# Performance work log

Measured on AMD Instinct MI355X. Metric: run time of the kernel, lower is better.

## Reference

```python
import jax, jax.numpy as jnp
import numpy as np
from jax import lax

K_NBR = 9  # K nearest neighbors
R = 2      # shuffle_scale


def pixel_unshuffle(x, r):
    B, C, H, W = x.shape
    x = x.reshape(B, C, H // r, r, W // r, r)
    return x.transpose(0, 1, 3, 5, 2, 4).reshape(B, C * r * r, H // r, W // r)


def pixel_shuffle(x, r):
    B, C, H, W = x.shape
    x = x.reshape(B, C // (r * r), r, r, H, W)
    return x.transpose(0, 1, 4, 2, 5, 3).reshape(B, C // (r * r), H * r, W * r)


def conv2d_same(x, w, b):
    y = lax.conv_general_dilated(x, w, (1, 1), 'SAME',
                                 dimension_numbers=('NCHW', 'OIHW', 'NCHW'))
    return y + b[None, :, None, None]


def convnn_branching_layer(x, idx, wa, ba, wb, bb, wp, bp):
    """Conv2d_ConvNN_Random_Branching with shuffle_pattern='BA'."""
    x = pixel_unshuffle(x, R)                      # (B, C*r^2, H/r, W/r)
    B, C, H, W = x.shape
    T = H * W
    # Branch 1: standard 3x3 conv
    y1 = conv2d_same(x, wa, ba)                    # (B, c1, H, W)
    # Branch 2: ConvNN on K nearest of N random samples
    xt = x.reshape(B, C, T)                        # tokens
    samp = xt[:, :, idx]                           # (B, C, N) random samples
    dots = jnp.einsum('bct,bcn->btn', xt, samp)
    xn = jnp.sum(xt * xt, axis=1)[:, :, None]      # (B, T, 1)
    sn = jnp.sum(samp * samp, axis=1)[:, None, :]  # (B, 1, N)
    dist = xn + sn - 2.0 * dots                    # squared euclidean (B, T, N)
    nbr = lax.top_k(-dist, K_NBR)[1]               # (B, T, K) indices into samples
    # gather neighbor features: (B, C, T*K)
    g = jnp.take_along_axis(samp, nbr.reshape(B, 1, T * K_NBR), axis=2)
    g = g.reshape(B, C, T, K_NBR)
    # Conv1d(kernel=K, stride=K) over stacked neighbors
    y2 = jnp.einsum('bctk,ock->bot', g, wb) + bb[None, :, None]
    y2 = y2.reshape(B, wb.shape[0], H, W)          # (B, c2, H, W)
    y = jax.nn.relu(jnp.concatenate([y1, y2], axis=1))
    y = conv2d_same(y, wp, bp)                     # 1x1 -> out*r^2 channels
    return pixel_shuffle(y, R)                     # (B, out, H*r, W*r)


def setup_inputs() -> dict:
    key = jax.random.key(0)
    ks = jax.random.split(key, 24)
    s = 0.02
    B = 256
    inp = {
        'x': jax.random.normal(ks[0], (B, 3, 32, 32), jnp.float32),
        'idx1': jax.random.randint(ks[1], (64,), 0, 256, jnp.int32),
        'idx2': jax.random.randint(ks[2], (64,), 0, 256, jnp.int32),
        # layer 1: Cin = 3*4 = 12, branches 16+16, out 16*4 = 64 pre-shuffle
        'w1a': jax.random.normal(ks[3], (16, 12, 3, 3), jnp.float32) * s,
        'b1a': jnp.zeros((16,), jnp.float32),
        'w1b': jax.random.normal(ks[4], (16, 12, 9), jnp.float32) * s,
        'b1b': jnp.zeros((16,), jnp.float32),
        'w1p': jax.random.normal(ks[5], (64, 32, 1, 1), jnp.float32) * s,
        'b1p': jnp.zeros((64,), jnp.float32),
        # layer 2: Cin = 16*4 = 64, branches 32+32, out 32*4 = 128 pre-shuffle
        'w2a': jax.random.normal(ks[6], (32, 64, 3, 3), jnp.float32) * s,
        'b2a': jnp.zeros((32,), jnp.float32),
        'w2b': jax.random.normal(ks[7], (32, 64, 9), jnp.float32) * s,
        'b2b': jnp.zeros((32,), jnp.float32),
        'w2p': jax.random.normal(ks[8], (128, 64, 1, 1), jnp.float32) * s,
        'b2p': jnp.zeros((128,), jnp.float32),
        # FC head
        'fc1w': jax.random.normal(ks[9], (1024, 32768), jnp.float32) * s,
        'fc1b': jnp.zeros((1024,), jnp.float32),
        'fc2w': jax.random.normal(ks[10], (10, 1024), jnp.float32) * s,
        'fc2b': jnp.zeros((10,), jnp.float32),
    }
    return inp


def reference(x, idx1, idx2, w1a, b1a, w1b, b1b, w1p, b1p,
              w2a, b2a, w2b, b2b, w2p, b2p, fc1w, fc1b, fc2w, fc2b):
    h = convnn_branching_layer(x, idx1, w1a, b1a, w1b, b1b, w1p, b1p)  # (B,16,32,32)
    h = convnn_branching_layer(h, idx2, w2a, b2a, w2b, b2b, w2p, b2p)  # (B,32,32,32)
    h = h.reshape(h.shape[0], -1)                   # (B, 32768)
    h = jax.nn.relu(h @ fc1w.T + fc1b)
    return h @ fc2w.T + fc2b                        # (B, num_classes)
```

## Files before the change

kernel.cpp:

```cpp
#include <hip/hip_runtime.h>
#include <cstdint>
#include <cstddef>


#define DI static __device__ __forceinline__

typedef __attribute__((ext_vector_type(8))) short short8;
typedef __attribute__((ext_vector_type(4))) float f32x4;

DI unsigned short f2bf(float v) {
  return __builtin_bit_cast(unsigned short, (__bf16)v);
}
DI float bf2f(unsigned short h) {
  return (float)__builtin_bit_cast(__bf16, h);
}

DI float xu1_at(const float* __restrict__ x, int b, int c, int t) {
  int h = t >> 4, w = t & 15;
  return x[(((size_t)b * 3 + (c >> 2)) * 32 + 2 * h + ((c >> 1) & 1)) * 32 + 2 * w + (c & 1)];
}

__global__ __launch_bounds__(256) void k_prepw(
    const float* __restrict__ w1b, float* __restrict__ wT1,
    const float* __restrict__ w2b, float* __restrict__ wT2,
    const float* __restrict__ w1p, float* __restrict__ wp1T,
    const float* __restrict__ w2p, float* __restrict__ wp2T,
    const float* __restrict__ w1a, float* __restrict__ wa1T,
    const float* __restrict__ w2a, float* __restrict__ wa2T)
{
  int i = blockIdx.x * 256 + threadIdx.x;
  if (i < 1728) {
    int k = i / 192, r = i % 192, c = r >> 4, o = r & 15;
    wT1[i] = w1b[((size_t)o * 12 + c) * 9 + k];
    return;
  }
  i -= 1728;
  if (i < 18432) {
    int k = i / 2048, r = i % 2048, c = r >> 5, o = r & 31;
    wT2[i] = w2b[((size_t)o * 64 + c) * 9 + k];
    return;
  }
  i -= 18432;
  if (i < 2048) { int ic = i >> 6, o = i & 63; wp1T[i] = w1p[(size_t)o * 32 + ic]; return; }
  i -= 2048;
  if (i < 8192) { int ic = i >> 7, o = i & 127; wp2T[i] = w2p[(size_t)o * 64 + ic]; return; }
  i -= 8192;
  if (i < 1728) {
    int o = i & 15, u = i >> 4, ic = u / 9, tp = u % 9;
    wa1T[i] = w1a[((size_t)o * 12 + ic) * 9 + tp];
    return;
  }
  i -= 1728;
  if (i < 18432) {
    int o = i & 31, u = i >> 5, ic = u / 9, tp = u % 9;
    wa2T[i] = w2a[((size_t)o * 64 + ic) * 9 + tp];
  }
}

template <int CIN, bool GATHER, int CCTOT, int OCT>
__global__ __launch_bounds__(256) void k_conv3x3(
    const float* __restrict__ xsrc, const float* __restrict__ xu,
    const float* __restrict__ waT, const float* __restrict__ bias,
    float* __restrict__ ycat)
{
  int b = blockIdx.x;
  int ocb = blockIdx.y * 16;
  __shared__ float xs[CIN * 256];
  int t = threadIdx.x;
  if (GATHER) {
    for (int i = t; i < CIN * 256; i += 256) {
      int c = i >> 8, tt = i & 255;
      xs[i] = xu1_at(xsrc, b, c, tt);
    }
  } else {
    for (int i = t; i < CIN * 256; i += 256) xs[i] = xu[(size_t)b * CIN * 256 + i];
  }
  __syncthreads();
  int tt = t & 127, og = t >> 7;
  int oc0 = ocb + og * 8;
  int h0 = tt >> 4, wc = tt & 15;
  float acc0[8], acc1[8];
#pragma unroll
  for (int o = 0; o < 8; ++o) { acc0[o] = bias[oc0 + o]; acc1[o] = acc0[o]; }
  bool vw0 = wc > 0, vw2 = wc < 15, vh0 = h0 > 0, vh7 = h0 < 7;
  bool m0v[9] = {vh0 && vw0, vh0, vh0 && vw2, vw0, true, vw2, vw0, true, vw2};
  bool m1v[9] = {vw0, true, vw2, vw0, true, vw2, vh7 && vw0, vh7, vh7 && vw2};
  int tc0[9], tc1[9];
#pragma unroll
  for (int dh = 0; dh < 3; ++dh)
#pragma unroll
    for (int dw = 0; dw < 3; ++dw) {
      int o0 = (h0 + dh - 1) * 16 + (wc + dw - 1);
      int o1 = (h0 + 8 + dh - 1) * 16 + (wc + dw - 1);
      tc0[dh * 3 + dw] = o0 < 0 ? 0 : (o0 > 255 ? 255 : o0);
      tc1[dh * 3 + dw] = o1 < 0 ? 0 : (o1 > 255 ? 255 : o1);
    }
#pragma unroll 2
  for (int ic = 0; ic < CIN; ++ic) {
    float xv0[9], xv1[9];
#pragma unroll
    for (int tp = 0; tp < 9; ++tp) {
      float v0 = xs[ic * 256 + tc0[tp]];
      float v1 = xs[ic * 256 + tc1[tp]];
      xv0[tp] = m0v[tp] ? v0 : 0.f;
      xv1[tp] = m1v[tp] ? v1 : 0.f;
    }
#pragma unroll
    for (int tp = 0; tp < 9; ++tp) {
      const float* wp = waT + ((size_t)ic * 9 + tp) * OCT + oc0;
      float4 wA = *(const float4*)wp;
      float4 wB = *(const float4*)(wp + 4);
      float wv[8] = {wA.x, wA.y, wA.z, wA.w, wB.x, wB.y, wB.z, wB.w};
#pragma unroll
      for (int o = 0; o < 8; ++o) {
        acc0[o] = fmaf(xv0[tp], wv[o], acc0[o]);
        acc1[o] = fmaf(xv1[tp], wv[o], acc1[o]);
      }
    }
  }
#pragma unroll
  for (int o = 0; o < 8; ++o) {
    ycat[((size_t)b * CCTOT + oc0 + o) * 256 + tt] = fmaxf(acc0[o], 0.f);
    ycat[((size_t)b * CCTOT + oc0 + o) * 256 + tt + 128] = fmaxf(acc1[o], 0.f);
  }
}

template <int C, bool GATHER, int OPT, int OTOT, int CCTOT, int OCBASE>
__global__ __launch_bounds__(256) void k_knn(
    const float* __restrict__ xsrc, const float* __restrict__ xu,
    const int* __restrict__ idx,
    const float* __restrict__ wT,
    const float* __restrict__ bb,
    float* __restrict__ ycat)
{
  int b = blockIdx.x, t = threadIdx.x;
  __shared__ float sph[C * 64];
  __shared__ float snvs[64];
  __shared__ int idxs[64];
  __shared__ int nbs[9 * 256];
  if (t < 64) idxs[t] = idx[t];
  __syncthreads();
  for (int i = t; i < C * 64; i += 256) {
    int c = i >> 6, n = i & 63;
    int p = idxs[n];
    sph[i] = GATHER ? xu1_at(xsrc, b, c, p) : xu[((size_t)b * C + c) * 256 + p];
  }
  __syncthreads();
  if (t < 64) {
    float s;
    {
#pragma clang fp contract(off)
      s = 0.f;
      for (int c = 0; c < C; ++c) { float v = sph[c * 64 + t]; s += v * v; }
    }
    snvs[t] = s;
  }
  float xcol[C];
#pragma unroll
  for (int c = 0; c < C; ++c)
    xcol[c] = GATHER ? xu1_at(xsrc, b, c, t) : xu[((size_t)b * C + c) * 256 + t];
  float xn;
  {
#pragma clang fp contract(off)
    xn = 0.f;
#pragma unroll
    for (int c = 0; c < C; ++c) xn += xcol[c] * xcol[c];
  }
  __syncthreads();
  float bd[9];
  int bn[9];
#pragma unroll
  for (int i = 0; i < 9; ++i) { bd[i] = __builtin_inff(); bn[i] = 1 << 30; }
#pragma unroll 1
  for (int n = 0; n < 64; ++n) {
    float snvn = snvs[n];
    float d;
    {
#pragma clang fp contract(off)
      float dot = 0.f;
#pragma unroll
      for (int c = 0; c < C; ++c) dot = fmaf(xcol[c], sph[c * 64 + n], dot);
      d = (xn + snvn) - 2.f * dot;
    }
    if (d < bd[8] || (d == bd[8] && n < bn[8])) {
      float dc = d;
      int nc = n;
#pragma unroll
      for (int i = 0; i < 9; ++i) {
        bool sw = (dc < bd[i]) || (dc == bd[i] && nc < bn[i]);
        float ob = bd[i]; int on = bn[i];
        bd[i] = sw ? dc : ob; bn[i] = sw ? nc : on;
        dc = sw ? ob : dc;   nc = sw ? on : nc;
      }
    }
  }
#pragma unroll
  for (int k = 0; k < 9; ++k) nbs[k * 256 + t] = bn[k];
  __syncthreads();
  int tt = t & 127, og = t >> 7;
  int o0 = og * OPT;
  int bnA[9], bnB[9];
#pragma unroll
  for (int k = 0; k < 9; ++k) {
    bnA[k] = nbs[k * 256 + tt];
    bnB[k] = nbs[k * 256 + tt + 128];
  }
  float acc0[OPT], acc1[OPT];
#pragma unroll
  for (int o = 0; o < OPT; ++o) { acc0[o] = bb[o0 + o]; acc1[o] = acc0[o]; }
#pragma unroll 1
  for (int k = 0; k < 9; ++k) {
    int n0 = bnA[k], n1 = bnB[k];
#pragma unroll 2
    for (int c = 0; c < C; ++c) {
      float sv0 = sph[c * 64 + n0];
      float sv1 = sph[c * 64 + n1];
      const float* wp = wT + ((size_t)k * C + c) * OTOT + o0;
#pragma unroll
      for (int oq = 0; oq < OPT / 4; ++oq) {
        float4 wv = ((const float4*)wp)[oq];
        float w4[4] = {wv.x, wv.y, wv.z, wv.w};
#pragma unroll
        for (int j = 0; j < 4; ++j) {
          acc0[oq * 4 + j] = fmaf(sv0, w4[j], acc0[oq * 4 + j]);
          acc1[oq * 4 + j] = fmaf(sv1, w4[j], acc1[oq * 4 + j]);
        }
      }
    }
  }
#pragma unroll
  for (int o = 0; o < OPT; ++o) {
    ycat[((size_t)b * CCTOT + OCBASE + o0 + o) * 256 + tt] = fmaxf(acc0[o], 0.f);
    ycat[((size_t)b * CCTOT + OCBASE + o0 + o) * 256 + tt + 128] = fmaxf(acc1[o], 0.f);
  }
}

template <int CIN, int OPT, int OCTOT, bool SHUF>
__global__ __launch_bounds__(256) void k_conv1x1(
    const float* __restrict__ yin, const float* __restrict__ wpT,
    const float* __restrict__ bias, float* __restrict__ out)
{
  int b = blockIdx.x, ocb = blockIdx.y * 2 * OPT, t = threadIdx.x;
  int tt = t & 127, og = t >> 7;
  int o0 = ocb + og * OPT;
  __shared__ float ys[CIN * 256];
  for (int i = t; i < CIN * 256; i += 256) ys[i] = yin[(size_t)b * CIN * 256 + i];
  __syncthreads();
  float acc0[OPT], acc1[OPT];
#pragma unroll
  for (int o = 0; o < OPT; ++o) { acc0[o] = bias[o0 + o]; acc1[o] = acc0[o]; }
#pragma unroll 2
  for (int ic = 0; ic < CIN; ++ic) {
    float sv0 = ys[ic * 256 + tt];
    float sv1 = ys[ic * 256 + tt + 128];
    const float* wp = wpT + (size_t)ic * OCTOT + o0;
#pragma unroll
    for (int oq = 0; oq < OPT / 4; ++oq) {
      float4 wv = ((const float4*)wp)[oq];
      float w4[4] = {wv.x, wv.y, wv.z, wv.w};
#pragma unroll
      for (int j = 0; j < 4; ++j) {
        acc0[oq * 4 + j] = fmaf(sv0, w4[j], acc0[oq * 4 + j]);
        acc1[oq * 4 + j] = fmaf(sv1, w4[j], acc1[oq * 4 + j]);
      }
    }
  }
  int h0 = tt >> 4, wc = tt & 15;
#pragma unroll
  for (int o = 0; o < OPT; ++o) {
    int ogl = o0 + o;
    if (SHUF) {
      int f0 = (ogl >> 2) * 1024 + (2 * h0 + ((ogl >> 1) & 1)) * 32 + (2 * wc + (ogl & 1));
      int f1 = (ogl >> 2) * 1024 + (2 * (h0 + 8) + ((ogl >> 1) & 1)) * 32 + (2 * wc + (ogl & 1));
      out[(size_t)b * 32768 + f0] = acc0[o];
      out[(size_t)b * 32768 + f1] = acc1[o];
    } else {
      out[((size_t)b * OCTOT + ogl) * 256 + tt] = acc0[o];
      out[((size_t)b * OCTOT + ogl) * 256 + tt + 128] = acc1[o];
    }
  }
}

__global__ __launch_bounds__(256, 2) void k_fc1(
    const float* __restrict__ A, const float* __restrict__ W,
    float* __restrict__ parts)
{
  constexpr int KTOT = 32768;
  constexpr int LDT = 36;
  __shared__ unsigned short Ah[128 * LDT], Am[128 * LDT], Al[128 * LDT];
  int t = threadIdx.x;
  int nb = blockIdx.x, mb = blockIdx.y, sb = blockIdx.z;
  int m0 = mb * 128, n0 = nb * 128, k0 = sb * 1024;
  int wave = t >> 6, lane = t & 63;
  int q = lane >> 4, m16 = lane & 15;

  f32x4 acc[8][2];
#pragma unroll
  for (int mt = 0; mt < 8; ++mt)
#pragma unroll
    for (int nt = 0; nt < 2; ++nt) acc[mt][nt] = (f32x4){0.f, 0.f, 0.f, 0.f};

  int arow = t >> 1, acol = (t & 1) * 16;
  const float* Ap = A + (size_t)(m0 + arow) * KTOT + k0 + acol;
  const float* W0 = W + (size_t)(n0 + wave * 32 + m16) * KTOT + k0 + q * 8;
  const float* W1 = W + (size_t)(n0 + wave * 32 + 16 + m16) * KTOT + k0 + q * 8;

  float4 aR0 = *(const float4*)(Ap + 0);
  float4 aR1 = *(const float4*)(Ap + 4);
  float4 aR2 = *(const float4*)(Ap + 8);
  float4 aR3 = *(const float4*)(Ap + 12);
  float4 w0a = *(const float4*)(W0), w0b = *(const float4*)(W0 + 4);
  float4 w1a = *(const float4*)(W1), w1b = *(const float4*)(W1 + 4);

  for (int ks = 0; ks < 1024; ks += 32) {
    int ksn = (ks + 32 < 1024) ? ks + 32 : 0;
    float4 nA0 = *(const float4*)(Ap + ksn);
    float4 nA1 = *(const float4*)(Ap + ksn + 4);
    float4 nA2 = *(const float4*)(Ap + ksn + 8);
    float4 nA3 = *(const float4*)(Ap + ksn + 12);
    float4 nW0a = *(const float4*)(W0 + ksn), nW0b = *(const float4*)(W0 + ksn + 4);
    float4 nW1a = *(const float4*)(W1 + ksn), nW1b = *(const float4*)(W1 + ksn + 4);

    short8 bh[2], bm[2], bl[2];
    {
      float wf0[8] = {w0a.x, w0a.y, w0a.z, w0a.w, w0b.x, w0b.y, w0b.z, w0b.w};
      float wf1[8] = {w1a.x, w1a.y, w1a.z, w1a.w, w1b.x, w1b.y, w1b.z, w1b.w};
#pragma unroll
      for (int j = 0; j < 8; ++j) {
        unsigned short h = f2bf(wf0[j]); float r1 = wf0[j] - bf2f(h);
        unsigned short m = f2bf(r1);
        bh[0][j] = (short)h; bm[0][j] = (short)m; bl[0][j] = (short)f2bf(r1 - bf2f(m));
        h = f2bf(wf1[j]); r1 = wf1[j] - bf2f(h);
        m = f2bf(r1);
        bh[1][j] = (short)h; bm[1][j] = (short)m; bl[1][j] = (short)f2bf(r1 - bf2f(m));
      }
    }
    short8 vh0, vh1, vm0, vm1, vl0, vl1;
    {
      float av[16] = {aR0.x, aR0.y, aR0.z, aR0.w, aR1.x, aR1.y, aR1.z, aR1.w,
                      aR2.x, aR2.y, aR2.z, aR2.w, aR3.x, aR3.y, aR3.z, aR3.w};
#pragma unroll
      for (int j = 0; j < 8; ++j) {
        {
          float v = av[j];
          unsigned short h = f2bf(v); float r1 = v - bf2f(h);
          unsigned short m = f2bf(r1);
          vh0[j] = (short)h; vm0[j] = (short)m; vl0[j] = (short)f2bf(r1 - bf2f(m));
        }
        {
          float v = av[j + 8];
          unsigned short h = f2bf(v); float r1 = v - bf2f(h);
          unsigned short m = f2bf(r1);
          vh1[j] = (short)h; vm1[j] = (short)m; vl1[j] = (short)f2bf(r1 - bf2f(m));
        }
      }
    }
    __syncthreads();
    {
      int off = arow * LDT + acol;
      *(short8*)&Ah[off] = vh0; *(short8*)&Ah[off + 8] = vh1;
      *(short8*)&Am[off] = vm0; *(short8*)&Am[off + 8] = vm1;
      *(short8*)&Al[off] = vl0; *(short8*)&Al[off + 8] = vl1;
    }
    __syncthreads();
#pragma unroll
    for (int mt = 0; mt < 8; ++mt) {
      int aoff = (mt * 16 + m16) * LDT + q * 8;
      short8 ah = *(const short8*)&Ah[aoff];
      short8 am = *(const short8*)&Am[aoff];
      short8 al = *(const short8*)&Al[aoff];
#pragma unroll
      for (int nt = 0; nt < 2; ++nt) {
        acc[mt][nt] = __builtin_amdgcn_mfma_f32_16x16x32_bf16(al, bh[nt], acc[mt][nt], 0, 0, 0);
        acc[mt][nt] = __builtin_amdgcn_mfma_f32_16x16x32_bf16(am, bm[nt], acc[mt][nt], 0, 0, 0);
        acc[mt][nt] = __builtin_amdgcn_mfma_f32_16x16x32_bf16(ah, bl[nt], acc[mt][nt], 0, 0, 0);
        acc[mt][nt] = __builtin_amdgcn_mfma_f32_16x16x32_bf16(am, bh[nt], acc[mt][nt], 0, 0, 0);
        acc[mt][nt] = __builtin_amdgcn_mfma_f32_16x16x32_bf16(ah, bm[nt], acc[mt][nt], 0, 0, 0);
        acc[mt][nt] = __builtin_amdgcn_mfma_f32_16x16x32_bf16(ah, bh[nt], acc[mt][nt], 0, 0, 0);
      }
    }
    aR0 = nA0; aR1 = nA1; aR2 = nA2; aR3 = nA3;
    w0a = nW0a; w0b = nW0b; w1a = nW1a; w1b = nW1b;
  }
  float* P = parts + (size_t)sb * 262144;
#pragma unroll
  for (int mt = 0; mt < 8; ++mt)
#pragma unroll
    for (int nt = 0; nt < 2; ++nt)
#pragma unroll
      for (int r2 = 0; r2 < 4; ++r2) {
        int m = m0 + mt * 16 + q * 4 + r2;
        int n = n0 + wave * 32 + nt * 16 + m16;
        P[(size_t)m * 1024 + n] = acc[mt][nt][r2];
      }
}

__global__ __launch_bounds__(256) void k_fc1_reduce(const float* __restrict__ parts,
                                                    const float* __restrict__ bias,
                                                    float* __restrict__ h1) {
  int i = blockIdx.x * 256 + threadIdx.x;
  float s = 0.f;
#pragma unroll
  for (int sb = 0; sb < 32; ++sb) s += parts[(size_t)sb * 262144 + i];
  h1[i] = fmaxf(s + bias[i & 1023], 0.f);
}

__global__ __launch_bounds__(256) void k_fc2(const float* __restrict__ h1,
                                             const float* __restrict__ w,
                                             const float* __restrict__ bias,
                                             float* __restrict__ out)
{
  int m = blockIdx.x, tid = threadIdx.x;
  __shared__ float hs[1024];
  __shared__ float ps[256];
  for (int i = tid; i < 1024; i += 256) hs[i] = h1[(size_t)m * 1024 + i];
  __syncthreads();
  int n = tid >> 4, sl = tid & 15;
  float p = 0.f;
  if (n < 10) {
    const float* wr = w + (size_t)n * 1024 + sl * 64;
    const float* hr = hs + sl * 64;
#pragma unroll 8
    for (int j = 0; j < 64; ++j) p = fmaf(hr[j], wr[j], p);
  }
  ps[tid] = p;
  __syncthreads();
  if (sl == 0 && n < 10) {
    float s = 0.f;
#pragma unroll
    for (int q = 0; q < 16; ++q) s += ps[n * 16 + q];
    out[(size_t)m * 10 + n] = s + bias[n];
  }
}

extern "C" void kernel_launch(void* const* d_in, const int* in_sizes, int n_in,
                              void* d_out, int out_size, void* d_ws, size_t ws_size,
                              hipStream_t stream) {
  (void)in_sizes; (void)n_in; (void)out_size; (void)ws_size;
  const float* x    = (const float*)d_in[0];
  const int*   idx1 = (const int*)d_in[1];
  const int*   idx2 = (const int*)d_in[2];
  const float* w1a  = (const float*)d_in[3];
  const float* b1a  = (const float*)d_in[4];
  const float* w1b  = (const float*)d_in[5];
  const float* b1b  = (const float*)d_in[6];
  const float* w1p  = (const float*)d_in[7];
  const float* b1p  = (const float*)d_in[8];
  const float* w2a  = (const float*)d_in[9];
  const float* b2a  = (const float*)d_in[10];
  const float* w2b  = (const float*)d_in[11];
  const float* b2b  = (const float*)d_in[12];
  const float* w2p  = (const float*)d_in[13];
  const float* b2p  = (const float*)d_in[14];
  const float* fc1w = (const float*)d_in[15];
  const float* fc1b = (const float*)d_in[16];
  const float* fc2w = (const float*)d_in[17];
  const float* fc2b = (const float*)d_in[18];

  float* ws    = (float*)d_ws;
  float* xu2   = ws + 0;
  float* ycat1 = ws + 4194304;
  float* ycat2 = ws + 4194304;
  float* WGT   = ws + 8388608;
  float* wT1   = WGT + 0;
  float* wT2   = WGT + 1728;
  float* wp1T  = WGT + 20160;
  float* wp2T  = WGT + 22208;
  float* wa1T  = WGT + 30400;
  float* wa2T  = WGT + 32128;
  float* h1    = ws + 8650752;
  float* hshuf = ws + 10485760;
  float* parts = ws + 0;
  float* out   = (float*)d_out;

  k_prepw<<<198, 256, 0, stream>>>(w1b, wT1, w2b, wT2, w1p, wp1T, w2p, wp2T, w1a, wa1T, w2a, wa2T);
  k_conv3x3<12, true, 32, 16><<<dim3(256, 1), 256, 0, stream>>>(x, nullptr, wa1T, b1a, ycat1);
  k_knn<12, true, 8, 16, 32, 16><<<256, 256, 0, stream>>>(x, nullptr, idx1, wT1, b1b, ycat1);
  k_conv1x1<32, 32, 64, false><<<dim3(256, 1), 256, 0, stream>>>(ycat1, wp1T, b1p, xu2);
  k_conv3x3<64, false, 64, 32><<<dim3(256, 2), 256, 0, stream>>>(nullptr, xu2, wa2T, b2a, ycat2);
  k_knn<64, false, 16, 32, 64, 32><<<256, 256, 0, stream>>>(nullptr, xu2, idx2, wT2, b2b, ycat2);
  k_conv1x1<64, 32, 128, true><<<dim3(256, 2), 256, 0, stream>>>(ycat2, wp2T, b2p, hshuf);
  k_fc1<<<dim3(8, 2, 32), 256, 0, stream>>>(hshuf, fc1w, parts);
  k_fc1_reduce<<<1024, 256, 0, stream>>>(parts, fc1b, h1);
  k_fc2<<<256, 256, 0, stream>>>(h1, fc2w, fc2b, out);
}
```

Before: 648.2 us.

## Split KNN kernel over pixel halves and sample groups with top-k merge

The KNN kernel now launches two blocks per batch image, each covering 128 pixels. Within a block, the two thread groups each scan half of the 64 samples and keep a partial top-9 list. The lists are merged through shared memory, and the group-split output-channel stage then handles one pixel per thread. This doubles the block count and halves the serial distance loop per thread, giving more parallelism for the latency-bound top-k scan. The cost is extra shared memory, a serial merge step run by only half the threads, and sample features loaded twice per image.

```diff
diff --git a/kernel.cpp b/kernel.cpp
--- a/kernel.cpp
+++ b/kernel.cpp
@@ -133,11 +133,13 @@
     const float* __restrict__ bb,
     float* __restrict__ ycat)
 {
-  int b = blockIdx.x, t = threadIdx.x;
+  int b = blockIdx.x, half = blockIdx.y, t = threadIdx.x;
   __shared__ float sph[C * 64];
   __shared__ float snvs[64];
   __shared__ int idxs[64];
-  __shared__ int nbs[9 * 256];
+  __shared__ float md[2][128][9];
+  __shared__ int mn_[2][128][9];
+  __shared__ int nbs[9 * 128];
   if (t < 64) idxs[t] = idx[t];
   __syncthreads();
   for (int i = t; i < C * 64; i += 256) {
@@ -155,10 +157,12 @@
     }
     snvs[t] = s;
   }
+  int tloc = t & 127, ng = t >> 7;
+  int px = half * 128 + tloc;
   float xcol[C];
 #pragma unroll
   for (int c = 0; c < C; ++c)
-    xcol[c] = GATHER ? xu1_at(xsrc, b, c, t) : xu[((size_t)b * C + c) * 256 + t];
+    xcol[c] = GATHER ? xu1_at(xsrc, b, c, px) : xu[((size_t)b * C + c) * 256 + px];
   float xn;
   {
 #pragma clang fp contract(off)
@@ -171,8 +175,8 @@
   int bn[9];
 #pragma unroll
   for (int i = 0; i < 9; ++i) { bd[i] = __builtin_inff(); bn[i] = 1 << 30; }
-#pragma unroll 1
-  for (int n = 0; n < 64; ++n) {
+#pragma unroll 2
+  for (int n = ng * 32; n < ng * 32 + 32; ++n) {
     float snvn = snvs[n];
     float d;
     {
@@ -195,44 +199,62 @@
     }
   }
 #pragma unroll
-  for (int k = 0; k < 9; ++k) nbs[k * 256 + t] = bn[k];
-  __syncthreads();
-  int tt = t & 127, og = t >> 7;
-  int o0 = og * OPT;
-  int bnA[9], bnB[9];
-#pragma unroll
-  for (int k = 0; k < 9; ++k) {
-    bnA[k] = nbs[k * 256 + tt];
-    bnB[k] = nbs[k * 256 + tt + 128];
-  }
-  float acc0[OPT], acc1[OPT];
-#pragma unroll
-  for (int o = 0; o < OPT; ++o) { acc0[o] = bb[o0 + o]; acc1[o] = acc0[o]; }
+  for (int k = 0; k < 9; ++k) { md[ng][tloc][k] = bd[k]; mn_[ng][tloc][k] = bn[k]; }
+  __syncthreads();
+  if (ng == 0) {
+    float fd[9];
+    int fn[9];
+#pragma unroll
+    for (int i = 0; i < 9; ++i) { fd[i] = __builtin_inff(); fn[i] = 1 << 30; }
+#pragma unroll 1
+    for (int gg = 0; gg < 2; ++gg)
+#pragma unroll
+      for (int k = 0; k < 9; ++k) {
+        float d = md[gg][tloc][k];
+        int n = mn_[gg][tloc][k];
+        if (d < fd[8] || (d == fd[8] && n < fn[8])) {
+          float dc = d;
+          int nc = n;
+#pragma unroll
+          for (int i = 0; i < 9; ++i) {
+            bool sw = (dc < fd[i]) || (dc == fd[i] && nc < fn[i]);
+            float ob = fd[i]; int on = fn[i];
+            fd[i] = sw ? dc : ob; fn[i] = sw ? nc : on;
+            dc = sw ? ob : dc;   nc = sw ? on : nc;
+          }
+        }
+      }
+#pragma unroll
+    for (int k = 0; k < 9; ++k) nbs[k * 128 + tloc] = fn[k];
+  }
+  __syncthreads();
+  int o0 = ng * OPT;
+  int bnA[9];
+#pragma unroll
+  for (int k = 0; k < 9; ++k) bnA[k] = nbs[k * 128 + tloc];
+  float acc0[OPT];
+#pragma unroll
+  for (int o = 0; o < OPT; ++o) acc0[o] = bb[o0 + o];
 #pragma unroll 1
   for (int k = 0; k < 9; ++k) {
-    int n0 = bnA[k], n1 = bnB[k];
+    int n0 = bnA[k];
 #pragma unroll 2
     for (int c = 0; c < C; ++c) {
       float sv0 = sph[c * 64 + n0];
-      float sv1 = sph[c * 64 + n1];
       const float* wp = wT + ((size_t)k * C + c) * OTOT + o0;
 #pragma unroll
       for (int oq = 0; oq < OPT / 4; ++oq) {
         float4 wv = ((const float4*)wp)[oq];
         float w4[4] = {wv.x, wv.y, wv.z, wv.w};
 #pragma unroll
-        for (int j = 0; j < 4; ++j) {
+        for (int j = 0; j < 4; ++j)
           acc0[oq * 4 + j] = fmaf(sv0, w4[j], acc0[oq * 4 + j]);
-          acc1[oq * 4 + j] = fmaf(sv1, w4[j], acc1[oq * 4 + j]);
-        }
-      }
-    }
-  }
-#pragma unroll
-  for (int o = 0; o < OPT; ++o) {
-    ycat[((size_t)b * CCTOT + OCBASE + o0 + o) * 256 + tt] = fmaxf(acc0[o], 0.f);
-    ycat[((size_t)b * CCTOT + OCBASE + o0 + o) * 256 + tt + 128] = fmaxf(acc1[o], 0.f);
-  }
+      }
+    }
+  }
+#pragma unroll
+  for (int o = 0; o < OPT; ++o)
+    ycat[((size_t)b * CCTOT + OCBASE + o0 + o) * 256 + px] = fmaxf(acc0[o], 0.f);
 }
 
 template <int CIN, int OPT, int OCTOT, bool SHUF>
@@ -475,10 +497,10 @@
 
   k_prepw<<<198, 256, 0, stream>>>(w1b, wT1, w2b, wT2, w1p, wp1T, w2p, wp2T, w1a, wa1T, w2a, wa2T);
   k_conv3x3<12, true, 32, 16><<<dim3(256, 1), 256, 0, stream>>>(x, nullptr, wa1T, b1a, ycat1);
-  k_knn<12, true, 8, 16, 32, 16><<<256, 256, 0, stream>>>(x, nullptr, idx1, wT1, b1b, ycat1);
+  k_knn<12, true, 8, 16, 32, 16><<<dim3(256, 2), 256, 0, stream>>>(x, nullptr, idx1, wT1, b1b, ycat1);
   k_conv1x1<32, 32, 64, false><<<dim3(256, 1), 256, 0, stream>>>(ycat1, wp1T, b1p, xu2);
   k_conv3x3<64, false, 64, 32><<<dim3(256, 2), 256, 0, stream>>>(nullptr, xu2, wa2T, b2a, ycat2);
-  k_knn<64, false, 16, 32, 64, 32><<<256, 256, 0, stream>>>(nullptr, xu2, idx2, wT2, b2b, ycat2);
+  k_knn<64, false, 16, 32, 64, 32><<<dim3(256, 2), 256, 0, stream>>>(nullptr, xu2, idx2, wT2, b2b, ycat2);
   k_conv1x1<64, 32, 128, true><<<dim3(256, 2), 256, 0, stream>>>(ycat2, wp2T, b2p, hshuf);
   k_fc1<<<dim3(8, 2, 32), 256, 0, stream>>>(hshuf, fc1w, parts);
   k_fc1_reduce<<<1024, 256, 0, stream>>>(parts, fc1b, h1);
```

After: 657.6 us. Within noise of the previous version (+1.5%).
